# Performance work log

Hardware: AMD Instinct MI355X
Metric: run time of the kernel (lower is better)

## Reference

```python
import jax, jax.numpy as jnp
import numpy as np

NUM_CLASSES = 60
NUM_HEADS = 8
TOP_M = 20
LN_EPS = 1e-5
NUM_LAYERS = 2


def setup_inputs() -> dict:
    key = jax.random.key(0)
    ks = jax.random.split(key, 13)
    D = 256  # feature_dim
    S = 72   # seq_len
    BNC = 32 * NUM_CLASSES  # batch * num_classes = 1920
    s = lambda k, shape, sc=0.02: jax.random.normal(k, shape, dtype=jnp.float32) * sc
    return {
        "reweighted_features": jax.random.normal(ks[0], (BNC, D, S), dtype=jnp.float32),
        "pos_embed": s(ks[1], (1, S, D)),
        # per-layer weights stacked on leading axis (L=2); Linear stored as (in, out)
        "qkv_w": s(ks[2], (NUM_LAYERS, D, 3 * D)),
        "qkv_b": jnp.zeros((NUM_LAYERS, 3 * D), dtype=jnp.float32),
        "proj_w": s(ks[3], (NUM_LAYERS, D, D)),
        "proj_b": jnp.zeros((NUM_LAYERS, D), dtype=jnp.float32),
        "ln_g": jnp.ones((NUM_LAYERS, D), dtype=jnp.float32),
        "ln_b": jnp.zeros((NUM_LAYERS, D), dtype=jnp.float32),
        "cls_w1": s(ks[4], (D, D // 2)),
        "cls_b1": jnp.zeros((D // 2,), dtype=jnp.float32),
        "cls_w2": s(ks[5], (D // 2, 1)),
        "cls_b2": jnp.zeros((1,), dtype=jnp.float32),
    }


def _layer_norm(x, g, b):
    mu = jnp.mean(x, axis=-1, keepdims=True)
    var = jnp.mean(jnp.square(x - mu), axis=-1, keepdims=True)
    return (x - mu) * jax.lax.rsqrt(var + LN_EPS) * g + b


def _topm_attention(x, qkv_w, qkv_b, proj_w, proj_b):
    B, N, C = x.shape
    hd = C // NUM_HEADS
    scale = hd ** -0.5
    qkv = (x @ qkv_w + qkv_b).reshape(B, N, 3, NUM_HEADS, hd)
    qkv = qkv.transpose(2, 0, 3, 1, 4)  # (3, B, H, N, hd)
    q, k, v = qkv[0], qkv[1], qkv[2]
    attn = jnp.einsum("bhnd,bhmd->bhnm", q, k) * scale  # (B, H, N, N)
    if TOP_M < N:
        # keep only the top-m scores per query row (ties negligible for random floats)
        topv = jax.lax.top_k(attn, TOP_M)[0]
        thr = topv[..., -1:]
        attn = jnp.where(attn >= thr, attn, -jnp.inf)
    p = jax.nn.softmax(attn, axis=-1)
    out = jnp.einsum("bhnm,bhmd->bhnd", p, v)
    out = out.transpose(0, 2, 1, 3).reshape(B, N, C)
    return out @ proj_w + proj_b


def reference(reweighted_features, pos_embed, qkv_w, qkv_b, proj_w, proj_b,
              ln_g, ln_b, cls_w1, cls_b1, cls_w2, cls_b2):
    BNC, D, S = reweighted_features.shape
    batch = BNC // NUM_CLASSES
    x = reweighted_features.transpose(0, 2, 1) + pos_embed  # (BNC, S, D)
    for i in range(NUM_LAYERS):
        x = x + _topm_attention(x, qkv_w[i], qkv_b[i], proj_w[i], proj_b[i])
        x = _layer_norm(x, ln_g[i], ln_b[i])
    x = x.mean(axis=1)  # (BNC, D)
    x = x.reshape(batch, NUM_CLASSES, D)
    h = jax.nn.relu(x @ cls_w1 + cls_b1)
    logits = (h @ cls_w2 + cls_b2)[..., 0]  # (batch, NUM_CLASSES)
    return logits
```

## Files before the change

kernel.cpp:

```cpp
#include <hip/hip_runtime.h>

#define NTOK 72
#define TOPM 20
#define GSEQ 4

typedef __attribute__((ext_vector_type(8))) short s8v;
typedef __attribute__((ext_vector_type(4))) float f4v;
typedef __attribute__((ext_vector_type(4))) unsigned short u16x4;

#define MFMA16(a, b, c) __builtin_amdgcn_mfma_f32_16x16x32_bf16((a), (b), (c), 0, 0, 0)

__device__ __forceinline__ unsigned short f2bf(float f) {
  unsigned int u = __float_as_uint(f);
  unsigned int r = (u + 0x7FFFu + ((u >> 16) & 1u)) >> 16;
  return (unsigned short)r;
}
__device__ __forceinline__ float bf2f(unsigned short s) {
  return __uint_as_float(((unsigned int)s) << 16);
}

__global__ void pack_w(const float* __restrict__ qkv_w, const float* __restrict__ proj_w,
                       const float* __restrict__ pos,
                       unsigned short* __restrict__ wq, unsigned short* __restrict__ wp,
                       unsigned short* __restrict__ posb) {
  int idx = blockIdx.x * 256 + threadIdx.x;
  if (idx < 2 * 768 * 256) {
    int k = idx & 255; int rest = idx >> 8; int j = rest % 768; int l = rest / 768;
    int h = j / 96, j96 = j - h * 96;
    int which = j96 >> 5, d = j96 & 31;
    wq[idx] = f2bf(qkv_w[(l * 256 + k) * 768 + which * 256 + h * 32 + d]);
  }
  if (idx < 2 * 256 * 256) {
    int k = idx & 255, n = (idx >> 8) & 255, l = idx >> 16;
    wp[idx] = f2bf(proj_w[(l * 256 + k) * 256 + n]);
  }
  if (idx < 72 * 256) posb[idx] = f2bf(pos[idx]);
}

__global__ __launch_bounds__(512, 2)
void k_qkv(const float* __restrict__ rf, const unsigned short* __restrict__ posb,
           unsigned short* __restrict__ xb,
           const unsigned short* __restrict__ wq,
           const float* __restrict__ qkv_b,
           unsigned short* __restrict__ qkvbuf,
           int layer, int b0)
{
  __shared__ __align__(16) unsigned short xs[80 * 264];
  __shared__ __align__(16) unsigned short st[256 * 72];
  const int tid = threadIdx.x, w = tid >> 6, l = tid & 63, q4 = l >> 4, l15 = l & 15;

  for (int i = tid; i < 80 * 264 / 2; i += 512) ((unsigned int*)xs)[i] = 0u;
  __syncthreads();

  const unsigned short* wqB = wq + (size_t)layer * 768 * 256;

  for (int g = 0; g < GSEQ; ++g) {
    const int b = blockIdx.x * GSEQ + g + b0;
    if (layer == 0) {
      const float* rfb = rf + (size_t)b * 18432;
      for (int i = tid; i < 18432; i += 512) {
        int c = i / 72, n = i - c * 72;
        float v = __builtin_nontemporal_load(rfb + i);
        xs[n * 264 + c] = f2bf(v + bf2f(posb[n * 256 + c]));
      }
    } else {
      const unsigned short* xbb = xb + (size_t)b * 18432;
      for (int i = tid; i < 2304; i += 512) {
        int n = i >> 5, c8 = (i & 31) << 3;
        s8v v = __builtin_nontemporal_load((const s8v*)(xbb + n * 256 + c8));
        *(s8v*)(xs + n * 264 + c8) = v;
      }
    }
    __syncthreads();
    if (layer == 0) {
      unsigned short* xbb = xb + (size_t)b * 18432;
      for (int i = tid; i < 2304; i += 512) {
        int n = i >> 5, c8 = (i & 31) << 3;
        __builtin_nontemporal_store(*(const s8v*)(xs + n * 264 + c8), (s8v*)(xbb + n * 256 + c8));
      }
    }

    unsigned short* qkvS = qkvbuf + (size_t)(b - b0) * 55296;
    for (int pass = 0; pass < 3; ++pass) {
      f4v acc[2][5];
      #pragma unroll
      for (int j = 0; j < 2; ++j)
        #pragma unroll
        for (int mt = 0; mt < 5; ++mt) acc[j][mt] = (f4v){0, 0, 0, 0};
      for (int kk = 0; kk < 8; ++kk) {
        int k0 = kk * 32 + q4 * 8;
        s8v a[5];
        #pragma unroll
        for (int mt = 0; mt < 5; ++mt) a[mt] = *(const s8v*)(xs + (mt * 16 + l15) * 264 + k0);
        #pragma unroll
        for (int j = 0; j < 2; ++j) {
          int jrow = pass * 256 + (w + 8 * j) * 16 + l15;
          s8v bf = *(const s8v*)(wqB + jrow * 256 + k0);
          #pragma unroll
          for (int mt = 0; mt < 5; ++mt) acc[j][mt] = MFMA16(a[mt], bf, acc[j][mt]);
        }
      }
      #pragma unroll
      for (int j = 0; j < 2; ++j) {
        int jl = (w + 8 * j) * 16 + l15;
        int j768 = pass * 256 + jl;
        int h = j768 / 96, j96 = j768 - h * 96;
        int which = j96 >> 5, d = j96 & 31;
        float bv = qkv_b[layer * 768 + which * 256 + h * 32 + d];
        float sc = (which == 0) ? 0.17677669529663687f : 1.0f;
        #pragma unroll
        for (int mt = 0; mt < 5; ++mt) {
          int tok0 = mt * 16 + q4 * 4;
          if (tok0 < NTOK) {
            u16x4 pk;
            #pragma unroll
            for (int r = 0; r < 4; ++r) pk[r] = f2bf((acc[j][mt][r] + bv) * sc);
            *(u16x4*)(st + jl * 72 + tok0) = pk;
          }
        }
      }
      __syncthreads();
      unsigned short* dst = qkvS + pass * 18432;
      for (int i = tid; i < 2304; i += 512)
        __builtin_nontemporal_store(*(const s8v*)(st + i * 8), (s8v*)(dst + i * 8));
      __syncthreads();
    }
  }
}

#define SP_S 104
__global__ __launch_bounds__(256, 4)
void k_attn(const unsigned short* __restrict__ qkvbuf, unsigned short* __restrict__ ohbuf,
            int b0)
{
  __shared__ __align__(16) unsigned short qs[80 * 40];
  __shared__ __align__(16) unsigned short ks[80 * 40];
  __shared__ __align__(16) unsigned short vt[32 * SP_S];
  __shared__ __align__(16) unsigned short sp[80 * SP_S];
  __shared__ __align__(16) unsigned short ostage[80 * 32];
  const int tid = threadIdx.x, w = tid >> 6, l = tid & 63, q4 = l >> 4, l15 = l & 15;
  const int bh = blockIdx.x;
  const int b = (bh >> 3) + b0, h = bh & 7;
  const unsigned short* qgq = qkvbuf + (size_t)(bh >> 3) * 55296 + (size_t)h * 96 * 72;
  const unsigned short* qgk = qgq + 32 * 72;
  const unsigned short* qgv = qgq + 64 * 72;

  for (int i = tid; i < 160; i += 256) ((unsigned int*)(qs + 72 * 40))[i] = 0u;
  for (int i = tid; i < 160; i += 256) ((unsigned int*)(ks + 72 * 40))[i] = 0u;
  for (int i = tid; i < 512; i += 256) {
    int d = i >> 4, c = (i & 15) << 1;
    *(unsigned int*)(vt + d * SP_S + 72 + c) = 0u;
  }
  for (int i = tid; i < 960; i += 256) {
    int rr = i / 12, c = (i % 12) << 1;
    *(unsigned int*)(sp + rr * SP_S + 80 + c) = 0u;
  }
  for (int i = tid; i < 1152; i += 256) {
    int f = i << 1;
    int d = f / 72, tok = f - d * 72;
    unsigned int v = __builtin_nontemporal_load((const unsigned int*)(qgq + f));
    qs[tok * 40 + d] = (unsigned short)v;
    qs[(tok + 1) * 40 + d] = (unsigned short)(v >> 16);
  }
  for (int i = tid; i < 1152; i += 256) {
    int f = i << 1;
    int d = f / 72, tok = f - d * 72;
    unsigned int v = __builtin_nontemporal_load((const unsigned int*)(qgk + f));
    ks[tok * 40 + d] = (unsigned short)v;
    ks[(tok + 1) * 40 + d] = (unsigned short)(v >> 16);
  }
  for (int i = tid; i < 288; i += 256) {
    int d = i / 9, t8 = (i - d * 9) << 3;
    s8v v = __builtin_nontemporal_load((const s8v*)(qgv + d * 72 + t8));
    *(s8v*)(vt + d * SP_S + t8) = v;
  }
  __syncthreads();

  for (int t = w; t < 25; t += 4) {
    int mt = t / 5, kt = t - mt * 5;
    s8v a  = *(const s8v*)(qs + (mt * 16 + l15) * 40 + q4 * 8);
    s8v bf = *(const s8v*)(ks + (kt * 16 + l15) * 40 + q4 * 8);
    f4v c = MFMA16(a, bf, ((f4v){0, 0, 0, 0}));
    int rowb = mt * 16 + q4 * 4, col = kt * 16 + l15;
    #pragma unroll
    for (int r = 0; r < 4; ++r) sp[(rowb + r) * SP_S + col] = f2bf(c[r]);
  }
  __syncthreads();

  for (int rp = 0; rp < 3; ++rp) {
    int row = rp * 32 + w * 8 + (l >> 3);
    if (row < NTOK) {
      int sub = l & 7;
      float vf[9]; unsigned int key[9];
      #pragma unroll
      for (int i = 0; i < 9; ++i) {
        unsigned int s = sp[row * SP_S + sub * 9 + i];
        vf[i] = bf2f((unsigned short)s);
        unsigned int m = (s >> 15) ? 0xFFFFu : 0x8000u;
        key[i] = s ^ m;
      }
      unsigned int thr = 0u;
      for (int bit = 15; bit >= 0; --bit) {
        unsigned int cand = thr | (1u << bit);
        int cnt = 0;
        #pragma unroll
        for (int i = 0; i < 9; ++i) cnt += (key[i] >= cand) ? 1 : 0;
        cnt += __shfl_xor(cnt, 1);
        cnt += __shfl_xor(cnt, 2);
        cnt += __shfl_xor(cnt, 4);
        if (cnt >= TOPM) thr = cand;
      }
      float mx = vf[0];
      #pragma unroll
      for (int i = 1; i < 9; ++i) mx = fmaxf(mx, vf[i]);
      mx = fmaxf(mx, __shfl_xor(mx, 1));
      mx = fmaxf(mx, __shfl_xor(mx, 2));
      mx = fmaxf(mx, __shfl_xor(mx, 4));
      float ssum = 0.f;
      #pragma unroll
      for (int i = 0; i < 9; ++i) {
        float e = (key[i] >= thr) ? __expf(vf[i] - mx) : 0.f;
        vf[i] = e; ssum += e;
      }
      ssum += __shfl_xor(ssum, 1);
      ssum += __shfl_xor(ssum, 2);
      ssum += __shfl_xor(ssum, 4);
      float inv = 1.f / ssum;
      #pragma unroll
      for (int i = 0; i < 9; ++i) sp[row * SP_S + sub * 9 + i] = f2bf(vf[i] * inv);
    }
  }
  __syncthreads();

  for (int t = w; t < 10; t += 4) {
    int mt = t >> 1, dt = t & 1;
    f4v acc = (f4v){0, 0, 0, 0};
    #pragma unroll
    for (int kk = 0; kk < 3; ++kk) {
      int k0 = kk * 32 + q4 * 8;
      s8v a  = *(const s8v*)(sp + (mt * 16 + l15) * SP_S + k0);
      s8v bf = *(const s8v*)(vt + (dt * 16 + l15) * SP_S + k0);
      acc = MFMA16(a, bf, acc);
    }
    int rowb = mt * 16 + q4 * 4, d = dt * 16 + l15;
    #pragma unroll
    for (int r = 0; r < 4; ++r) ostage[(rowb + r) * 32 + d] = f2bf(acc[r]);
  }
  __syncthreads();

  unsigned short* ohb = ohbuf + (size_t)b * 18432 + h * 32;
  for (int i = tid; i < 288; i += 256) {
    int tok = i >> 2, c8 = (i & 3) << 3;
    __builtin_nontemporal_store(*(const s8v*)(ostage + tok * 32 + c8), (s8v*)(ohb + tok * 256 + c8));
  }
}

__global__ __launch_bounds__(512, 2)
void k_proj(const unsigned short* __restrict__ ohbuf, const unsigned short* __restrict__ wp,
            const float* __restrict__ proj_b, const float* __restrict__ ln_g,
            const float* __restrict__ ln_b,
            unsigned short* __restrict__ xb,
            const float* __restrict__ w1, const float* __restrict__ b1,
            const float* __restrict__ w2, const float* __restrict__ b2,
            float* __restrict__ out, int layer, int last)
{
  __shared__ __align__(16) unsigned short os[80 * 264];
  __shared__ float red[160];
  __shared__ float mbufs[GSEQ][256];
  __shared__ float hb[GSEQ][128];
  const int tid = threadIdx.x, w = tid >> 6, l = tid & 63, q4 = l >> 4, l15 = l & 15;

  for (int i = tid; i < 80 * 264 / 2; i += 512) ((unsigned int*)os)[i] = 0u;
  for (int i = tid; i < GSEQ * 256; i += 512) ((float*)mbufs)[i] = 0.f;
  if (tid < GSEQ * 128) ((float*)hb)[tid] = 0.f;
  __syncthreads();

  const unsigned short* wpB = wp + (size_t)layer * 65536;
  const int c0 = w * 32 + l15, c1 = c0 + 16;
  const float pb0 = proj_b[layer * 256 + c0], pb1 = proj_b[layer * 256 + c1];
  const float g0 = ln_g[layer * 256 + c0], g1 = ln_g[layer * 256 + c1];
  const float be0 = ln_b[layer * 256 + c0], be1 = ln_b[layer * 256 + c1];

  for (int g = 0; g < GSEQ; ++g) {
    const int b = blockIdx.x * GSEQ + g;
    const unsigned short* ohb = ohbuf + (size_t)b * 18432;
    for (int i = tid; i < 2304; i += 512) {
      int n = i >> 5, c8 = (i & 31) << 3;
      s8v v = __builtin_nontemporal_load((const s8v*)(ohb + n * 256 + c8));
      *(s8v*)(os + n * 264 + c8) = v;
    }
    if (tid < 160) red[tid] = 0.f;
    __syncthreads();

    f4v acc[5][2];
    #pragma unroll
    for (int mt = 0; mt < 5; ++mt) { acc[mt][0] = (f4v){0,0,0,0}; acc[mt][1] = (f4v){0,0,0,0}; }
    for (int kk = 0; kk < 8; ++kk) {
      int k0 = kk * 32 + q4 * 8;
      s8v a[5];
      #pragma unroll
      for (int mt = 0; mt < 5; ++mt) a[mt] = *(const s8v*)(os + (mt * 16 + l15) * 264 + k0);
      #pragma unroll
      for (int j = 0; j < 2; ++j) {
        int nrow = w * 32 + j * 16 + l15;
        s8v bf = *(const s8v*)(wpB + nrow * 256 + k0);
        #pragma unroll
        for (int mt = 0; mt < 5; ++mt) acc[mt][j] = MFMA16(a[mt], bf, acc[mt][j]);
      }
    }

    const unsigned short* xbb = xb + (size_t)b * 18432;
    #pragma unroll
    for (int mt = 0; mt < 5; ++mt) {
      #pragma unroll
      for (int r = 0; r < 4; ++r) {
        int row = mt * 16 + q4 * 4 + r;
        float z0 = 0.f, z1 = 0.f;
        if (row < NTOK) {
          z0 = bf2f(xbb[row * 256 + c0]) + acc[mt][0][r] + pb0;
          z1 = bf2f(xbb[row * 256 + c1]) + acc[mt][1][r] + pb1;
        }
        acc[mt][0][r] = z0; acc[mt][1][r] = z1;
        float s1 = z0 + z1, s2 = z0 * z0 + z1 * z1;
        s1 += __shfl_xor(s1, 1); s2 += __shfl_xor(s2, 1);
        s1 += __shfl_xor(s1, 2); s2 += __shfl_xor(s2, 2);
        s1 += __shfl_xor(s1, 4); s2 += __shfl_xor(s2, 4);
        s1 += __shfl_xor(s1, 8); s2 += __shfl_xor(s2, 8);
        if (l15 == 0 && row < NTOK) {
          atomicAdd(&red[row * 2], s1);
          atomicAdd(&red[row * 2 + 1], s2);
        }
      }
    }
    __syncthreads();

    float msum0 = 0.f, msum1 = 0.f;
    #pragma unroll
    for (int mt = 0; mt < 5; ++mt) {
      #pragma unroll
      for (int r = 0; r < 4; ++r) {
        int row = mt * 16 + q4 * 4 + r;
        if (row < NTOK) {
          float mu = red[row * 2] * (1.f / 256.f);
          float var = red[row * 2 + 1] * (1.f / 256.f) - mu * mu;
          float rstd = rsqrtf(var + 1e-5f);
          float o0 = (acc[mt][0][r] - mu) * rstd * g0 + be0;
          float o1 = (acc[mt][1][r] - mu) * rstd * g1 + be1;
          if (!last) {
            os[row * 264 + c0] = f2bf(o0);
            os[row * 264 + c1] = f2bf(o1);
          } else {
            msum0 += o0; msum1 += o1;
          }
        }
      }
    }
    if (last) {
      atomicAdd(&mbufs[g][c0], msum0);
      atomicAdd(&mbufs[g][c1], msum1);
    }
    __syncthreads();
    if (!last) {
      unsigned short* xbw = xb + (size_t)b * 18432;
      for (int i = tid; i < 2304; i += 512) {
        int n = i >> 5, c8 = (i & 31) << 3;
        __builtin_nontemporal_store(*(const s8v*)(os + n * 264 + c8), (s8v*)(xbw + n * 256 + c8));
      }
    }
    __syncthreads();
  }

  if (last) {
    {
      int col = tid & 127, kq = tid >> 7;
      float sums[GSEQ];
      #pragma unroll
      for (int g = 0; g < GSEQ; ++g) sums[g] = 0.f;
      for (int k = kq * 64; k < kq * 64 + 64; ++k) {
        float wv = w1[k * 128 + col] * (1.f / 72.f);
        #pragma unroll
        for (int g = 0; g < GSEQ; ++g) sums[g] += mbufs[g][k] * wv;
      }
      #pragma unroll
      for (int g = 0; g < GSEQ; ++g) atomicAdd(&hb[g][col], sums[g]);
    }
    __syncthreads();
    if (w == 0) {
      #pragma unroll
      for (int g = 0; g < GSEQ; ++g) {
        float h0 = fmaxf(hb[g][l] + b1[l], 0.f);
        float h1 = fmaxf(hb[g][l + 64] + b1[l + 64], 0.f);
        float p = h0 * w2[l] + h1 * w2[l + 64];
        p += __shfl_xor(p, 1);  p += __shfl_xor(p, 2);  p += __shfl_xor(p, 4);
        p += __shfl_xor(p, 8);  p += __shfl_xor(p, 16); p += __shfl_xor(p, 32);
        if (l == 0) out[blockIdx.x * GSEQ + g] = p + b2[0];
      }
    }
  }
}

extern "C" void kernel_launch(void* const* d_in, const int* in_sizes, int n_in,
                              void* d_out, int out_size, void* d_ws, size_t ws_size,
                              hipStream_t stream) {
  const float* rf    = (const float*)d_in[0];
  const float* pos   = (const float*)d_in[1];
  const float* qkvw  = (const float*)d_in[2];
  const float* qkvb  = (const float*)d_in[3];
  const float* projw = (const float*)d_in[4];
  const float* projb = (const float*)d_in[5];
  const float* lng   = (const float*)d_in[6];
  const float* lnb   = (const float*)d_in[7];
  const float* w1    = (const float*)d_in[8];
  const float* b1    = (const float*)d_in[9];
  const float* w2    = (const float*)d_in[10];
  const float* b2    = (const float*)d_in[11];
  float* out = (float*)d_out;

  unsigned short* wq   = (unsigned short*)d_ws;
  unsigned short* wp   = wq + 393216;
  unsigned short* posb = wp + 131072;
  unsigned short* xb   = posb + 18432;
  unsigned short* oh   = xb + 35389440;
  unsigned short* qkv  = oh + 35389440;

  const size_t fixed_bytes = (size_t)(393216 + 131072 + 18432 + 35389440 + 35389440) * 2;
  const size_t qkv_bytes   = (size_t)1920 * 768 * 72 * 2;
  int nc = 1;
  while (nc < 8 && fixed_bytes + qkv_bytes / nc > ws_size) nc *= 2;
  const int bc = 1920 / nc;

  hipLaunchKernelGGL(pack_w, dim3(1536), dim3(256), 0, stream, qkvw, projw, pos, wq, wp, posb);
  for (int layer = 0; layer < 2; ++layer) {
    for (int c = 0; c < nc; ++c) {
      int b0 = c * bc;
      hipLaunchKernelGGL(k_qkv, dim3(bc / GSEQ), dim3(512), 0, stream,
                         rf, posb, xb, wq, qkvb, qkv, layer, b0);
      hipLaunchKernelGGL(k_attn, dim3(bc * 8), dim3(256), 0, stream, qkv, oh, b0);
    }
    hipLaunchKernelGGL(k_proj, dim3(1920 / GSEQ), dim3(512), 0, stream,
                       oh, wp, projb, lng, lnb, xb, w1, b1, w2, b2, out,
                       layer, layer == 1 ? 1 : 0);
  }
}
```

Baseline: 1.549 ms.

## Store Q/K token-major and vectorize top-m softmax with ballot counting

The QKV projection swaps MFMA operands for the Q and K groups so they are written token-major (tok*32+d) per head. The attention kernel can then load them with 16-byte vector loads instead of scalar transposing scatters into LDS. The top-m threshold search now counts with __ballot plus popcount instead of three shuffle-add reductions. Each row's 72 scores are read and written as one 8-wide vector per lane plus one scalar, and the output staging buffer aliases qs to cut LDS use. The price is a more branchy epilogue in the QKV kernel and a changed intermediate layout that both kernels must agree on.

New measurement: 1.409 ms. 9.0% less time.

```diff
diff --git a/kernel.cpp b/kernel.cpp
--- a/kernel.cpp
+++ b/kernel.cpp
@@ -82,40 +82,70 @@
 
     unsigned short* qkvS = qkvbuf + (size_t)(b - b0) * 55296;
     for (int pass = 0; pass < 3; ++pass) {
+      int jb[2], j768b[2], hh[2], j96b[2], whg[2];
+      #pragma unroll
+      for (int jj = 0; jj < 2; ++jj) {
+        jb[jj] = (w + 8 * jj) * 16;
+        j768b[jj] = pass * 256 + jb[jj];
+        hh[jj] = j768b[jj] / 96;
+        j96b[jj] = j768b[jj] - hh[jj] * 96;
+        whg[jj] = j96b[jj] >> 5;
+      }
       f4v acc[2][5];
       #pragma unroll
-      for (int j = 0; j < 2; ++j)
-        #pragma unroll
-        for (int mt = 0; mt < 5; ++mt) acc[j][mt] = (f4v){0, 0, 0, 0};
+      for (int jj = 0; jj < 2; ++jj)
+        #pragma unroll
+        for (int mt = 0; mt < 5; ++mt) acc[jj][mt] = (f4v){0, 0, 0, 0};
       for (int kk = 0; kk < 8; ++kk) {
         int k0 = kk * 32 + q4 * 8;
         s8v a[5];
         #pragma unroll
         for (int mt = 0; mt < 5; ++mt) a[mt] = *(const s8v*)(xs + (mt * 16 + l15) * 264 + k0);
         #pragma unroll
-        for (int j = 0; j < 2; ++j) {
-          int jrow = pass * 256 + (w + 8 * j) * 16 + l15;
-          s8v bf = *(const s8v*)(wqB + jrow * 256 + k0);
+        for (int jj = 0; jj < 2; ++jj) {
+          s8v bw = *(const s8v*)(wqB + (j768b[jj] + l15) * 256 + k0);
+          if (whg[jj] < 2) {
+            #pragma unroll
+            for (int mt = 0; mt < 5; ++mt) acc[jj][mt] = MFMA16(bw, a[mt], acc[jj][mt]);
+          } else {
+            #pragma unroll
+            for (int mt = 0; mt < 5; ++mt) acc[jj][mt] = MFMA16(a[mt], bw, acc[jj][mt]);
+          }
+        }
+      }
+      #pragma unroll
+      for (int jj = 0; jj < 2; ++jj) {
+        int gg = jb[jj] >> 5;
+        unsigned short* stg = st + gg * 2304;
+        if (whg[jj] < 2) {
+          int dloc = (j96b[jj] & 31) + q4 * 4;
+          float scl = (whg[jj] == 0) ? 0.17677669529663687f : 1.0f;
+          float bv[4];
           #pragma unroll
-          for (int mt = 0; mt < 5; ++mt) acc[j][mt] = MFMA16(a[mt], bf, acc[j][mt]);
-        }
-      }
-      #pragma unroll
-      for (int j = 0; j < 2; ++j) {
-        int jl = (w + 8 * j) * 16 + l15;
-        int j768 = pass * 256 + jl;
-        int h = j768 / 96, j96 = j768 - h * 96;
-        int which = j96 >> 5, d = j96 & 31;
-        float bv = qkv_b[layer * 768 + which * 256 + h * 32 + d];
-        float sc = (which == 0) ? 0.17677669529663687f : 1.0f;
-        #pragma unroll
-        for (int mt = 0; mt < 5; ++mt) {
-          int tok0 = mt * 16 + q4 * 4;
-          if (tok0 < NTOK) {
-            u16x4 pk;
-            #pragma unroll
-            for (int r = 0; r < 4; ++r) pk[r] = f2bf((acc[j][mt][r] + bv) * sc);
-            *(u16x4*)(st + jl * 72 + tok0) = pk;
+          for (int r = 0; r < 4; ++r)
+            bv[r] = qkv_b[layer * 768 + whg[jj] * 256 + hh[jj] * 32 + dloc + r];
+          #pragma unroll
+          for (int mt = 0; mt < 5; ++mt) {
+            int tok = mt * 16 + l15;
+            if (tok < NTOK) {
+              u16x4 pk;
+              #pragma unroll
+              for (int r = 0; r < 4; ++r) pk[r] = f2bf((acc[jj][mt][r] + bv[r]) * scl);
+              *(u16x4*)(stg + tok * 32 + dloc) = pk;
+            }
+          }
+        } else {
+          int d = (j96b[jj] & 31) + l15;
+          float bv = qkv_b[layer * 768 + 512 + hh[jj] * 32 + d];
+          #pragma unroll
+          for (int mt = 0; mt < 5; ++mt) {
+            int tok0 = mt * 16 + q4 * 4;
+            if (tok0 < NTOK) {
+              u16x4 pk;
+              #pragma unroll
+              for (int r = 0; r < 4; ++r) pk[r] = f2bf(acc[jj][mt][r] + bv);
+              *(u16x4*)(stg + d * 72 + tok0) = pk;
+            }
           }
         }
       }
@@ -137,13 +167,13 @@
   __shared__ __align__(16) unsigned short ks[80 * 40];
   __shared__ __align__(16) unsigned short vt[32 * SP_S];
   __shared__ __align__(16) unsigned short sp[80 * SP_S];
-  __shared__ __align__(16) unsigned short ostage[80 * 32];
+  unsigned short* ostage = qs;
   const int tid = threadIdx.x, w = tid >> 6, l = tid & 63, q4 = l >> 4, l15 = l & 15;
   const int bh = blockIdx.x;
   const int b = (bh >> 3) + b0, h = bh & 7;
-  const unsigned short* qgq = qkvbuf + (size_t)(bh >> 3) * 55296 + (size_t)h * 96 * 72;
-  const unsigned short* qgk = qgq + 32 * 72;
-  const unsigned short* qgv = qgq + 64 * 72;
+  const unsigned short* qgq = qkvbuf + (size_t)(bh >> 3) * 55296 + (size_t)h * 6912;
+  const unsigned short* qgk = qgq + 2304;
+  const unsigned short* qgv = qgq + 4608;
 
   for (int i = tid; i < 160; i += 256) ((unsigned int*)(qs + 72 * 40))[i] = 0u;
   for (int i = tid; i < 160; i += 256) ((unsigned int*)(ks + 72 * 40))[i] = 0u;
@@ -155,19 +185,15 @@
     int rr = i / 12, c = (i % 12) << 1;
     *(unsigned int*)(sp + rr * SP_S + 80 + c) = 0u;
   }
-  for (int i = tid; i < 1152; i += 256) {
-    int f = i << 1;
-    int d = f / 72, tok = f - d * 72;
-    unsigned int v = __builtin_nontemporal_load((const unsigned int*)(qgq + f));
-    qs[tok * 40 + d] = (unsigned short)v;
-    qs[(tok + 1) * 40 + d] = (unsigned short)(v >> 16);
-  }
-  for (int i = tid; i < 1152; i += 256) {
-    int f = i << 1;
-    int d = f / 72, tok = f - d * 72;
-    unsigned int v = __builtin_nontemporal_load((const unsigned int*)(qgk + f));
-    ks[tok * 40 + d] = (unsigned short)v;
-    ks[(tok + 1) * 40 + d] = (unsigned short)(v >> 16);
+  for (int i = tid; i < 288; i += 256) {
+    int tok = i >> 2, d8 = (i & 3) << 3;
+    s8v v = __builtin_nontemporal_load((const s8v*)(qgq + tok * 32 + d8));
+    *(s8v*)(qs + tok * 40 + d8) = v;
+  }
+  for (int i = tid; i < 288; i += 256) {
+    int tok = i >> 2, d8 = (i & 3) << 3;
+    s8v v = __builtin_nontemporal_load((const s8v*)(qgk + tok * 32 + d8));
+    *(s8v*)(ks + tok * 40 + d8) = v;
   }
   for (int i = tid; i < 288; i += 256) {
     int d = i / 9, t8 = (i - d * 9) << 3;
@@ -187,27 +213,33 @@
   }
   __syncthreads();
 
+  const int rowsh = l & 56;
   for (int rp = 0; rp < 3; ++rp) {
     int row = rp * 32 + w * 8 + (l >> 3);
     if (row < NTOK) {
       int sub = l & 7;
+      unsigned short* rowp = sp + row * SP_S;
+      s8v raw = *(const s8v*)(rowp + sub * 8);
+      unsigned short uv[9];
+      #pragma unroll
+      for (int i = 0; i < 8; ++i) uv[i] = (unsigned short)raw[i];
+      uv[8] = rowp[64 + sub];
       float vf[9]; unsigned int key[9];
       #pragma unroll
       for (int i = 0; i < 9; ++i) {
-        unsigned int s = sp[row * SP_S + sub * 9 + i];
+        unsigned int s = uv[i];
         vf[i] = bf2f((unsigned short)s);
-        unsigned int m = (s >> 15) ? 0xFFFFu : 0x8000u;
-        key[i] = s ^ m;
+        key[i] = s ^ ((s >> 15) ? 0xFFFFu : 0x8000u);
       }
       unsigned int thr = 0u;
       for (int bit = 15; bit >= 0; --bit) {
         unsigned int cand = thr | (1u << bit);
         int cnt = 0;
         #pragma unroll
-        for (int i = 0; i < 9; ++i) cnt += (key[i] >= cand) ? 1 : 0;
-        cnt += __shfl_xor(cnt, 1);
-        cnt += __shfl_xor(cnt, 2);
-        cnt += __shfl_xor(cnt, 4);
+        for (int i = 0; i < 9; ++i) {
+          unsigned long long m = __ballot(key[i] >= cand);
+          cnt += __popc((unsigned int)(m >> rowsh) & 0xffu);
+        }
         if (cnt >= TOPM) thr = cand;
       }
       float mx = vf[0];
@@ -226,8 +258,11 @@
       ssum += __shfl_xor(ssum, 2);
       ssum += __shfl_xor(ssum, 4);
       float inv = 1.f / ssum;
-      #pragma unroll
-      for (int i = 0; i < 9; ++i) sp[row * SP_S + sub * 9 + i] = f2bf(vf[i] * inv);
+      s8v pout;
+      #pragma unroll
+      for (int i = 0; i < 8; ++i) pout[i] = (short)f2bf(vf[i] * inv);
+      *(s8v*)(rowp + sub * 8) = pout;
+      rowp[64 + sub] = f2bf(vf[8] * inv);
     }
   }
   __syncthreads();
```
